# Kernel tuning notes

Measured on AMD Instinct MI355X. Metric: run time of the kernel, lower is better.

Reference implementation:

```python
import jax, jax.numpy as jnp
import numpy as np

NUM_NODES = 100000
NUM_EDGES = 600000
NUM_GRAPHS = 1000
EMB = 128


def setup_inputs() -> dict:
    key = jax.random.key(0)
    ks = jax.random.split(key, 12)
    x = jax.random.normal(ks[0], (NUM_NODES, 4), dtype=jnp.float32)
    edge_index = jax.random.randint(ks[1], (2, NUM_EDGES), 0, NUM_NODES, dtype=jnp.int32)
    x_scalar = jax.random.normal(ks[2], (NUM_GRAPHS, 4), dtype=jnp.float32)
    batch_index = jnp.sort(jax.random.randint(ks[3], (NUM_NODES,), 0, NUM_GRAPHS, dtype=jnp.int32))
    def glorot(k, shape):
        fan_in, fan_out = shape[0], shape[1]
        s = jnp.sqrt(2.0 / (fan_in + fan_out)).astype(jnp.float32)
        return jax.random.normal(k, shape, dtype=jnp.float32) * s
    return {
        "x": x,
        "edge_index": edge_index,
        "x_scalar": x_scalar,
        "batch_index": batch_index,
        "W0": glorot(ks[4], (4, EMB)), "b0": jnp.zeros((EMB,), jnp.float32),
        "W1": glorot(ks[5], (EMB, EMB)), "b1": jnp.zeros((EMB,), jnp.float32),
        "W2": glorot(ks[6], (EMB, EMB)), "b2": jnp.zeros((EMB,), jnp.float32),
        "W3": glorot(ks[7], (EMB, EMB)), "b3": jnp.zeros((EMB,), jnp.float32),
        "Wl1": glorot(ks[8], (EMB + 4, 64)), "bl1": jnp.zeros((64,), jnp.float32),
        "Wl2": glorot(ks[9], (64, 1)), "bl2": jnp.zeros((1,), jnp.float32),
    }


def _gcn_norm(edge_index, num_nodes):
    # PyG GCNConv default: add self-loops, symmetric normalization
    loop = jnp.arange(num_nodes, dtype=edge_index.dtype)
    src = jnp.concatenate([edge_index[0], loop])
    dst = jnp.concatenate([edge_index[1], loop])
    deg = jax.ops.segment_sum(jnp.ones_like(src, dtype=jnp.float32), dst,
                              num_segments=num_nodes)
    dinv = jnp.where(deg > 0, jax.lax.rsqrt(jnp.maximum(deg, 1e-12)), 0.0)
    norm = dinv[src] * dinv[dst]  # [E+N]
    return src, dst, norm


def _gcn_conv(h, src, dst, norm, W, b, num_nodes):
    h = h @ W                                   # [N, out]
    msg = h[src] * norm[:, None]                # gather + normalize
    out = jax.ops.segment_sum(msg, dst, num_segments=num_nodes)  # scatter-add
    return out + b


def reference(x, edge_index, x_scalar, batch_index,
              W0, b0, W1, b1, W2, b2, W3, b3, Wl1, bl1, Wl2, bl2):
    n = x.shape[0]
    src, dst, norm = _gcn_norm(edge_index, n)
    h = jax.nn.relu(_gcn_conv(x, src, dst, norm, W0, b0, n))
    h = jax.nn.relu(_gcn_conv(h, src, dst, norm, W1, b1, n))
    h = jax.nn.relu(_gcn_conv(h, src, dst, norm, W2, b2, n))
    h = jax.nn.relu(_gcn_conv(h, src, dst, norm, W3, b3, n))
    # global mean pool over batch_index
    sums = jax.ops.segment_sum(h, batch_index, num_segments=NUM_GRAPHS)
    cnts = jax.ops.segment_sum(jnp.ones((n,), jnp.float32), batch_index,
                               num_segments=NUM_GRAPHS)
    pooled = sums / jnp.maximum(cnts, 1.0)[:, None]          # [G, EMB]
    feat = jnp.concatenate([pooled, x_scalar], axis=1)       # [G, EMB+4]
    out = jax.nn.relu(feat @ Wl1 + bl1) @ Wl2 + bl2          # [G, 1]
    return out
```

## Files before the change

kernel.cpp:

```cpp
#include <hip/hip_runtime.h>

#define NN 100000
#define EE 600000
#define GG 1000
#define NB ((NN + 255) / 256)

typedef __bf16 bf16x8 __attribute__((ext_vector_type(8)));
typedef float f32x4 __attribute__((ext_vector_type(4)));
typedef unsigned int u32;

__device__ inline float2 bf2_to_f2(u32 u) {
  return make_float2(__uint_as_float(u << 16), __uint_as_float(u & 0xffff0000u));
}
__device__ inline u32 f2_to_bf2(float a, float b) {
  union { __bf16 h[2]; u32 u; } pk;
  pk.h[0] = (__bf16)a; pk.h[1] = (__bf16)b;
  return pk.u;
}


__global__ void k_init(int* cnt, int* fillc, int* gstart) {
  int i = blockIdx.x * 256 + threadIdx.x;
  if (i < NN) { cnt[i] = 0; fillc[i] = 0; }
  if (i <= GG) gstart[i] = NN;
}

__global__ void k_count(const int* __restrict__ dst, int* cnt) {
  int e = blockIdx.x * 256 + threadIdx.x;
  if (e < EE) atomicAdd(&cnt[dst[e]], 1);
}

__global__ void k_scan1(const int* __restrict__ cnt, float* __restrict__ dinv,
                        int* rowptr, int* bsum) {
  __shared__ int s[256];
  int tid = threadIdx.x;
  int i = blockIdx.x * 256 + tid;
  int v = (i < NN) ? ((cnt[i] + 7) & ~7) : 0;
  if (i < NN) dinv[i] = rsqrtf((float)(cnt[i] + 1));
  s[tid] = v;
  __syncthreads();
  for (int off = 1; off < 256; off <<= 1) {
    int t = (tid >= off) ? s[tid - off] : 0;
    __syncthreads();
    s[tid] += t;
    __syncthreads();
  }
  if (i <= NN) rowptr[i] = s[tid] - v;
  if (tid == 255) bsum[blockIdx.x] = s[255];
}

__global__ void k_scan2(int* bsum) {
  __shared__ int s[512];
  int tid = threadIdx.x;
  int v = (tid < NB) ? bsum[tid] : 0;
  s[tid] = v;
  __syncthreads();
  for (int off = 1; off < 512; off <<= 1) {
    int t = (tid >= off) ? s[tid - off] : 0;
    __syncthreads();
    s[tid] += t;
    __syncthreads();
  }
  if (tid < NB) bsum[tid] = s[tid] - v;
}

__global__ void k_scan3(int* rowptr, const int* __restrict__ bsum) {
  int i = blockIdx.x * 256 + threadIdx.x;
  if (i <= NN) rowptr[i] += bsum[blockIdx.x];
}

__global__ void k_fillpad(const int* __restrict__ src, const int* __restrict__ dst,
                          const int* __restrict__ rowptr, int* fillc,
                          const int* __restrict__ cnt,
                          const float* __restrict__ dinv,
                          int2* __restrict__ csr) {
  int gid = blockIdx.x * 256 + threadIdx.x;
  if (gid < EE) {
    int s = src[gid], d = dst[gid];
    int pos = rowptr[d] + atomicAdd(&fillc[d], 1);
    csr[pos] = make_int2(s, __float_as_int(dinv[s] * dinv[d]));
  }
  if (gid < NN) {
    int2 pad = make_int2(gid, 0);
    for (int pos = rowptr[gid] + cnt[gid]; pos < rowptr[gid + 1]; ++pos)
      csr[pos] = pad;
  }
}

__global__ void k_gbound(const int* __restrict__ batch, int* gstart) {
  int i = blockIdx.x * 256 + threadIdx.x;
  if (i >= NN) return;
  int b = batch[i];
  if (i == 0) {
    for (int g = 0; g <= b; ++g) gstart[g] = 0;
  } else {
    int prev = batch[i - 1];
    for (int g = prev + 1; g <= b; ++g) gstart[g] = i;
  }
}

__global__ void k_wprep(const float* __restrict__ W, __bf16* __restrict__ Wt) {
  int idx = blockIdx.x * 256 + threadIdx.x;
  int n = idx >> 7, k = idx & 127;
  Wt[(size_t)n * 128 + k] = (__bf16)W[(size_t)k * 128 + n];
}


__global__ void k_mm0(const float* __restrict__ x, const float* __restrict__ W0,
                      __bf16* __restrict__ hout) {
  int idx = blockIdx.x * 256 + threadIdx.x;
  if (idx >= NN * 128) return;
  int node = idx >> 7, j = idx & 127;
  const float* xr = x + node * 4;
  float s = xr[0] * W0[j];
  s = fmaf(xr[1], W0[128 + j], s);
  s = fmaf(xr[2], W0[256 + j], s);
  s = fmaf(xr[3], W0[384 + j], s);
  hout[idx] = (__bf16)s;
}

#define LDSPAD 136
__global__ __launch_bounds__(256) void k_mfma(const __bf16* __restrict__ hin,
                                              const __bf16* __restrict__ Wt,
                                              __bf16* __restrict__ hout) {
  __shared__ __bf16 As[128 * LDSPAD];
  int tid = threadIdx.x;
  int row0 = blockIdx.x * 128;
  int lane = tid & 63, w = tid >> 6;
  int ln = lane & 15, quad = lane >> 4;

  bf16x8 bfrag[8][4];
  #pragma unroll
  for (int nt = 0; nt < 8; ++nt)
    #pragma unroll
    for (int kc = 0; kc < 4; ++kc)
      bfrag[nt][kc] = *(const bf16x8*)(Wt + (size_t)(nt * 16 + ln) * 128 + kc * 32 + quad * 8);

  #pragma unroll
  for (int i = 0; i < 8; ++i) {
    int eb = (i * 256 + tid) * 8;
    int r = eb >> 7, c = eb & 127;
    int gr = row0 + r;
    uint4 v = make_uint4(0, 0, 0, 0);
    if (gr < NN) v = *(const uint4*)(hin + (size_t)gr * 128 + c);
    *(uint4*)&As[r * LDSPAD + c] = v;
  }
  __syncthreads();

  f32x4 acc[2][8];
  #pragma unroll
  for (int rt = 0; rt < 2; ++rt)
    #pragma unroll
    for (int nt = 0; nt < 8; ++nt) acc[rt][nt] = (f32x4){0.f, 0.f, 0.f, 0.f};

  #pragma unroll
  for (int kc = 0; kc < 4; ++kc) {
    bf16x8 a0 = *(const bf16x8*)&As[(w * 32 + ln) * LDSPAD + kc * 32 + quad * 8];
    bf16x8 a1 = *(const bf16x8*)&As[(w * 32 + 16 + ln) * LDSPAD + kc * 32 + quad * 8];
    #pragma unroll
    for (int nt = 0; nt < 8; ++nt) {
      acc[0][nt] = __builtin_amdgcn_mfma_f32_16x16x32_bf16(a0, bfrag[nt][kc], acc[0][nt], 0, 0, 0);
      acc[1][nt] = __builtin_amdgcn_mfma_f32_16x16x32_bf16(a1, bfrag[nt][kc], acc[1][nt], 0, 0, 0);
    }
  }

  #pragma unroll
  for (int rt = 0; rt < 2; ++rt)
    #pragma unroll
    for (int nt = 0; nt < 8; ++nt)
      #pragma unroll
      for (int reg = 0; reg < 4; ++reg) {
        int gr = row0 + w * 32 + rt * 16 + quad * 4 + reg;
        if (gr < NN)
          hout[(size_t)gr * 128 + nt * 16 + ln] = (__bf16)acc[rt][nt][reg];
      }
}

__global__ __launch_bounds__(256) void k_aggregate(const __bf16* __restrict__ hlin,
                                                   const int* __restrict__ rowptr,
                                                   const int2* __restrict__ csr,
                                                   const float* __restrict__ dinv,
                                                   const float* __restrict__ bias,
                                                   u32* __restrict__ hout2) {
  int node = blockIdx.x * 4 + (threadIdx.x >> 6);
  int lane = threadIdx.x & 63;
  int ln = lane & 15, quad = lane >> 4;
  if (node >= NN) return;
  float di = dinv[node];
  float sw = di * di;

  uint4 su = *(const uint4*)(hlin + ((size_t)node << 7) + ln * 8);
  float4 ba = *(const float4*)(bias + ln * 8);
  float4 bb = *(const float4*)(bias + ln * 8 + 4);
  float2 s0 = bf2_to_f2(su.x), s1 = bf2_to_f2(su.y);
  float2 s2 = bf2_to_f2(su.z), s3 = bf2_to_f2(su.w);
  float q0 = (quad == 0) ? 1.f : 0.f;
  float acc[8];
  acc[0] = q0 * fmaf(sw, s0.x, ba.x); acc[1] = q0 * fmaf(sw, s0.y, ba.y);
  acc[2] = q0 * fmaf(sw, s1.x, ba.z); acc[3] = q0 * fmaf(sw, s1.y, ba.w);
  acc[4] = q0 * fmaf(sw, s2.x, bb.x); acc[5] = q0 * fmaf(sw, s2.y, bb.y);
  acc[6] = q0 * fmaf(sw, s3.x, bb.z); acc[7] = q0 * fmaf(sw, s3.y, bb.w);

  int beg = rowptr[node], end = rowptr[node + 1];
  for (int base = beg; base < end; base += 64) {
    int m = end - base; if (m > 64) m = 64;
    int li = base + (lane < m ? lane : m - 1);
    int2 md = csr[li];
    int idxv = md.x, wbits = md.y;
    for (int j = 0; j < m; j += 8) {
      int sl0 = (j + quad) * 4, sl1 = (j + 4 + quad) * 4;
      int r0 = __builtin_amdgcn_ds_bpermute(sl0, idxv);
      int r1 = __builtin_amdgcn_ds_bpermute(sl1, idxv);
      float w0 = __int_as_float(__builtin_amdgcn_ds_bpermute(sl0, wbits));
      float w1 = __int_as_float(__builtin_amdgcn_ds_bpermute(sl1, wbits));
      uint4 u0 = *(const uint4*)(hlin + ((size_t)r0 << 7) + ln * 8);
      uint4 u1 = *(const uint4*)(hlin + ((size_t)r1 << 7) + ln * 8);
      float2 f;
      f = bf2_to_f2(u0.x); acc[0] = fmaf(w0, f.x, acc[0]); acc[1] = fmaf(w0, f.y, acc[1]);
      f = bf2_to_f2(u0.y); acc[2] = fmaf(w0, f.x, acc[2]); acc[3] = fmaf(w0, f.y, acc[3]);
      f = bf2_to_f2(u0.z); acc[4] = fmaf(w0, f.x, acc[4]); acc[5] = fmaf(w0, f.y, acc[5]);
      f = bf2_to_f2(u0.w); acc[6] = fmaf(w0, f.x, acc[6]); acc[7] = fmaf(w0, f.y, acc[7]);
      f = bf2_to_f2(u1.x); acc[0] = fmaf(w1, f.x, acc[0]); acc[1] = fmaf(w1, f.y, acc[1]);
      f = bf2_to_f2(u1.y); acc[2] = fmaf(w1, f.x, acc[2]); acc[3] = fmaf(w1, f.y, acc[3]);
      f = bf2_to_f2(u1.z); acc[4] = fmaf(w1, f.x, acc[4]); acc[5] = fmaf(w1, f.y, acc[5]);
      f = bf2_to_f2(u1.w); acc[6] = fmaf(w1, f.x, acc[6]); acc[7] = fmaf(w1, f.y, acc[7]);
    }
  }

  #pragma unroll
  for (int k = 0; k < 8; ++k) {
    acc[k] += __shfl_xor(acc[k], 16);
    acc[k] += __shfl_xor(acc[k], 32);
  }
  if (quad == 0) {
    uint4 o;
    o.x = f2_to_bf2(fmaxf(acc[0], 0.f), fmaxf(acc[1], 0.f));
    o.y = f2_to_bf2(fmaxf(acc[2], 0.f), fmaxf(acc[3], 0.f));
    o.z = f2_to_bf2(fmaxf(acc[4], 0.f), fmaxf(acc[5], 0.f));
    o.w = f2_to_bf2(fmaxf(acc[6], 0.f), fmaxf(acc[7], 0.f));
    *(uint4*)(hout2 + (size_t)node * 64 + ln * 4) = o;
  }
}

__global__ __launch_bounds__(256) void k_poolmlp(const uint2* __restrict__ h4u,
                                                 const int* __restrict__ gstart,
                                                 const float* __restrict__ xs,
                                                 const float* __restrict__ Wl1,
                                                 const float* __restrict__ bl1,
                                                 const float* __restrict__ Wl2,
                                                 const float* __restrict__ bl2,
                                                 float* __restrict__ out) {
  __shared__ float4 part[8][32];
  __shared__ float pooled[128];
  int g = blockIdx.x;
  int beg = gstart[g], end = gstart[g + 1];
  int tid = threadIdx.x;
  int cg = tid & 31;
  int rg = tid >> 5;
  float4 acc = make_float4(0.f, 0.f, 0.f, 0.f);
  for (int i = beg + rg; i < end; i += 8) {
    uint2 u = h4u[(size_t)i * 32 + cg];
    acc.x += __uint_as_float(u.x << 16);
    acc.y += __uint_as_float(u.x & 0xffff0000u);
    acc.z += __uint_as_float(u.y << 16);
    acc.w += __uint_as_float(u.y & 0xffff0000u);
  }
  part[rg][cg] = acc;
  __syncthreads();
  if (tid < 32) {
    float4 s = part[0][tid];
    #pragma unroll
    for (int r = 1; r < 8; ++r) {
      float4 v = part[r][tid];
      s.x += v.x; s.y += v.y; s.z += v.z; s.w += v.w;
    }
    float sc = 1.f / fmaxf((float)(end - beg), 1.f);
    pooled[tid * 4 + 0] = s.x * sc;
    pooled[tid * 4 + 1] = s.y * sc;
    pooled[tid * 4 + 2] = s.z * sc;
    pooled[tid * 4 + 3] = s.w * sc;
  }
  __syncthreads();
  if (tid < 64) {
    float hj = bl1[tid];
    #pragma unroll 4
    for (int k = 0; k < 128; ++k) hj = fmaf(pooled[k], Wl1[k * 64 + tid], hj);
    const float* xr = xs + g * 4;
    #pragma unroll
    for (int k = 0; k < 4; ++k) hj = fmaf(xr[k], Wl1[(128 + k) * 64 + tid], hj);
    hj = fmaxf(hj, 0.f);
    float val = hj * Wl2[tid];
    #pragma unroll
    for (int off = 32; off > 0; off >>= 1) val += __shfl_down(val, off);
    if (tid == 0) out[g] = val + bl2[0];
  }
}


extern "C" void kernel_launch(void* const* d_in, const int* in_sizes, int n_in,
                              void* d_out, int out_size, void* d_ws, size_t ws_size,
                              hipStream_t stream) {
  const float* x    = (const float*)d_in[0];
  const int*   ei   = (const int*)d_in[1];
  const float* xs   = (const float*)d_in[2];
  const int*   batch= (const int*)d_in[3];
  const float* W0   = (const float*)d_in[4];
  const float* b0   = (const float*)d_in[5];
  const float* W1   = (const float*)d_in[6];
  const float* b1   = (const float*)d_in[7];
  const float* W2   = (const float*)d_in[8];
  const float* b2   = (const float*)d_in[9];
  const float* W3   = (const float*)d_in[10];
  const float* b3   = (const float*)d_in[11];
  const float* Wl1  = (const float*)d_in[12];
  const float* bl1  = (const float*)d_in[13];
  const float* Wl2  = (const float*)d_in[14];
  const float* bl2  = (const float*)d_in[15];
  const int* srcA = ei;
  const int* dstA = ei + EE;
  float* out = (float*)d_out;

  char* p = (char*)d_ws;
  auto take = [&](size_t bytes) { char* q = p; p += (bytes + 255) & ~(size_t)255; return q; };
  __bf16* hA   = (__bf16*)take((size_t)NN * 128 * 2);
  __bf16* hB   = (__bf16*)take((size_t)NN * 128 * 2);
  int*   cnt   = (int*)take((size_t)NN * 4);
  float* dinv  = (float*)take((size_t)NN * 4);
  int*   rowptr= (int*)take((size_t)(NN + 1) * 4);
  int*   fillc = (int*)take((size_t)NN * 4);
  int2*  csr   = (int2*)take((size_t)(EE + 7 * NN + 64) * 8);
  int*   bsum  = (int*)take(512 * 4);
  int*   gstart= (int*)take((size_t)(GG + 1) * 4);
  __bf16* Wt1  = (__bf16*)take(16384 * 2);
  __bf16* Wt2  = (__bf16*)take(16384 * 2);
  __bf16* Wt3  = (__bf16*)take(16384 * 2);

  k_init<<<NB, 256, 0, stream>>>(cnt, fillc, gstart);
  k_count<<<(EE + 255) / 256, 256, 0, stream>>>(dstA, cnt);
  k_scan1<<<NB, 256, 0, stream>>>(cnt, dinv, rowptr, bsum);
  k_scan2<<<1, 512, 0, stream>>>(bsum);
  k_scan3<<<NB, 256, 0, stream>>>(rowptr, bsum);
  k_fillpad<<<(EE + 255) / 256, 256, 0, stream>>>(srcA, dstA, rowptr, fillc, cnt, dinv, csr);
  k_gbound<<<NB, 256, 0, stream>>>(batch, gstart);
  k_wprep<<<64, 256, 0, stream>>>(W1, Wt1);
  k_wprep<<<64, 256, 0, stream>>>(W2, Wt2);
  k_wprep<<<64, 256, 0, stream>>>(W3, Wt3);

  k_mm0<<<(NN * 128 + 255) / 256, 256, 0, stream>>>(x, W0, hA);
  k_aggregate<<<(NN + 3) / 4, 256, 0, stream>>>(hA, rowptr, csr, dinv, b0, (u32*)hB);
  k_mfma<<<(NN + 127) / 128, 256, 0, stream>>>(hB, Wt1, hA);
  k_aggregate<<<(NN + 3) / 4, 256, 0, stream>>>(hA, rowptr, csr, dinv, b1, (u32*)hB);
  k_mfma<<<(NN + 127) / 128, 256, 0, stream>>>(hB, Wt2, hA);
  k_aggregate<<<(NN + 3) / 4, 256, 0, stream>>>(hA, rowptr, csr, dinv, b2, (u32*)hB);
  k_mfma<<<(NN + 127) / 128, 256, 0, stream>>>(hB, Wt3, hA);
  k_aggregate<<<(NN + 3) / 4, 256, 0, stream>>>(hA, rowptr, csr, dinv, b3, (u32*)hB);

  k_poolmlp<<<GG, 256, 0, stream>>>((const uint2*)hB, gstart, xs, Wl1, bl1, Wl2, bl2, out);
}
```

Baseline: 414.2 us.

## Aggregate before linear transform so first layer gathers 4-wide input

Reorders each GCN layer to aggregate neighbours first and then apply the weight matrix, moving bias and ReLU into the MFMA epilogue. The first layer now gathers the 4-feature input instead of 128-wide transformed features, removing one full 128-wide sparse aggregation pass. Setup kernels for CSR fill, graph bounds and weight transposes are merged into one launch. Rounding points for bf16 intermediates change slightly.

```diff
diff --git a/kernel.cpp b/kernel.cpp
--- a/kernel.cpp
+++ b/kernel.cpp
@@ -69,11 +69,16 @@
   if (i <= NN) rowptr[i] += bsum[blockIdx.x];
 }
 
-__global__ void k_fillpad(const int* __restrict__ src, const int* __restrict__ dst,
-                          const int* __restrict__ rowptr, int* fillc,
-                          const int* __restrict__ cnt,
-                          const float* __restrict__ dinv,
-                          int2* __restrict__ csr) {
+__global__ void k_setup2(const int* __restrict__ src, const int* __restrict__ dst,
+                         const int* __restrict__ rowptr, int* fillc,
+                         const int* __restrict__ cnt,
+                         const float* __restrict__ dinv,
+                         int2* __restrict__ csr,
+                         const int* __restrict__ batch, int* gstart,
+                         const float* __restrict__ W1, const float* __restrict__ W2,
+                         const float* __restrict__ W3,
+                         __bf16* __restrict__ Wt1, __bf16* __restrict__ Wt2,
+                         __bf16* __restrict__ Wt3) {
   int gid = blockIdx.x * 256 + threadIdx.x;
   if (gid < EE) {
     int s = src[gid], d = dst[gid];
@@ -84,44 +89,64 @@
     int2 pad = make_int2(gid, 0);
     for (int pos = rowptr[gid] + cnt[gid]; pos < rowptr[gid + 1]; ++pos)
       csr[pos] = pad;
-  }
-}
-
-__global__ void k_gbound(const int* __restrict__ batch, int* gstart) {
+    int b = batch[gid];
+    if (gid == 0) {
+      for (int g = 0; g <= b; ++g) gstart[g] = 0;
+    } else {
+      int prev = batch[gid - 1];
+      for (int g = prev + 1; g <= b; ++g) gstart[g] = gid;
+    }
+  }
+  if (gid < 3 * 16384) {
+    int which = gid >> 14, idx = gid & 16383;
+    int n = idx >> 7, k = idx & 127;
+    const float* W = (which == 0) ? W1 : (which == 1) ? W2 : W3;
+    __bf16* Wt = (which == 0) ? Wt1 : (which == 1) ? Wt2 : Wt3;
+    Wt[(size_t)n * 128 + k] = (__bf16)W[(size_t)k * 128 + n];
+  }
+}
+
+
+__global__ void k_aggx(const float4* __restrict__ x, const int* __restrict__ rowptr,
+                       const int* __restrict__ cnt, const int2* __restrict__ csr,
+                       const float* __restrict__ dinv, float4* __restrict__ y) {
   int i = blockIdx.x * 256 + threadIdx.x;
   if (i >= NN) return;
-  int b = batch[i];
-  if (i == 0) {
-    for (int g = 0; g <= b; ++g) gstart[g] = 0;
-  } else {
-    int prev = batch[i - 1];
-    for (int g = prev + 1; g <= b; ++g) gstart[g] = i;
-  }
-}
-
-__global__ void k_wprep(const float* __restrict__ W, __bf16* __restrict__ Wt) {
-  int idx = blockIdx.x * 256 + threadIdx.x;
-  int n = idx >> 7, k = idx & 127;
-  Wt[(size_t)n * 128 + k] = (__bf16)W[(size_t)k * 128 + n];
-}
-
-
-__global__ void k_mm0(const float* __restrict__ x, const float* __restrict__ W0,
-                      __bf16* __restrict__ hout) {
+  float di = dinv[i];
+  float sw = di * di;
+  float4 xi = x[i];
+  float4 acc = make_float4(sw * xi.x, sw * xi.y, sw * xi.z, sw * xi.w);
+  int beg = rowptr[i], end = beg + cnt[i];
+  for (int e = beg; e < end; ++e) {
+    int2 md = csr[e];
+    float w = __int_as_float(md.y);
+    float4 v = x[md.x];
+    acc.x = fmaf(w, v.x, acc.x);
+    acc.y = fmaf(w, v.y, acc.y);
+    acc.z = fmaf(w, v.z, acc.z);
+    acc.w = fmaf(w, v.w, acc.w);
+  }
+  y[i] = acc;
+}
+
+__global__ void k_lin0(const float4* __restrict__ y, const float* __restrict__ W0,
+                       const float* __restrict__ b0, __bf16* __restrict__ hout) {
   int idx = blockIdx.x * 256 + threadIdx.x;
   if (idx >= NN * 128) return;
   int node = idx >> 7, j = idx & 127;
-  const float* xr = x + node * 4;
-  float s = xr[0] * W0[j];
-  s = fmaf(xr[1], W0[128 + j], s);
-  s = fmaf(xr[2], W0[256 + j], s);
-  s = fmaf(xr[3], W0[384 + j], s);
-  hout[idx] = (__bf16)s;
+  float4 yv = y[node];
+  float s = b0[j];
+  s = fmaf(yv.x, W0[j], s);
+  s = fmaf(yv.y, W0[128 + j], s);
+  s = fmaf(yv.z, W0[256 + j], s);
+  s = fmaf(yv.w, W0[384 + j], s);
+  hout[idx] = (__bf16)fmaxf(s, 0.f);
 }
 
 #define LDSPAD 136
 __global__ __launch_bounds__(256) void k_mfma(const __bf16* __restrict__ hin,
                                               const __bf16* __restrict__ Wt,
+                                              const float* __restrict__ bias,
                                               __bf16* __restrict__ hout) {
   __shared__ __bf16 As[128 * LDSPAD];
   int tid = threadIdx.x;
@@ -130,11 +155,14 @@
   int ln = lane & 15, quad = lane >> 4;
 
   bf16x8 bfrag[8][4];
-  #pragma unroll
-  for (int nt = 0; nt < 8; ++nt)
+  float bcol[8];
+  #pragma unroll
+  for (int nt = 0; nt < 8; ++nt) {
+    bcol[nt] = bias[nt * 16 + ln];
     #pragma unroll
     for (int kc = 0; kc < 4; ++kc)
       bfrag[nt][kc] = *(const bf16x8*)(Wt + (size_t)(nt * 16 + ln) * 128 + kc * 32 + quad * 8);
+  }
 
   #pragma unroll
   for (int i = 0; i < 8; ++i) {
@@ -172,7 +200,8 @@
       for (int reg = 0; reg < 4; ++reg) {
         int gr = row0 + w * 32 + rt * 16 + quad * 4 + reg;
         if (gr < NN)
-          hout[(size_t)gr * 128 + nt * 16 + ln] = (__bf16)acc[rt][nt][reg];
+          hout[(size_t)gr * 128 + nt * 16 + ln] =
+              (__bf16)fmaxf(acc[rt][nt][reg] + bcol[nt], 0.f);
       }
 }
 
@@ -180,7 +209,6 @@
                                                    const int* __restrict__ rowptr,
                                                    const int2* __restrict__ csr,
                                                    const float* __restrict__ dinv,
-                                                   const float* __restrict__ bias,
                                                    u32* __restrict__ hout2) {
   int node = blockIdx.x * 4 + (threadIdx.x >> 6);
   int lane = threadIdx.x & 63;
@@ -190,16 +218,14 @@
   float sw = di * di;
 
   uint4 su = *(const uint4*)(hlin + ((size_t)node << 7) + ln * 8);
-  float4 ba = *(const float4*)(bias + ln * 8);
-  float4 bb = *(const float4*)(bias + ln * 8 + 4);
   float2 s0 = bf2_to_f2(su.x), s1 = bf2_to_f2(su.y);
   float2 s2 = bf2_to_f2(su.z), s3 = bf2_to_f2(su.w);
-  float q0 = (quad == 0) ? 1.f : 0.f;
+  float q0 = (quad == 0) ? sw : 0.f;
   float acc[8];
-  acc[0] = q0 * fmaf(sw, s0.x, ba.x); acc[1] = q0 * fmaf(sw, s0.y, ba.y);
-  acc[2] = q0 * fmaf(sw, s1.x, ba.z); acc[3] = q0 * fmaf(sw, s1.y, ba.w);
-  acc[4] = q0 * fmaf(sw, s2.x, bb.x); acc[5] = q0 * fmaf(sw, s2.y, bb.y);
-  acc[6] = q0 * fmaf(sw, s3.x, bb.z); acc[7] = q0 * fmaf(sw, s3.y, bb.w);
+  acc[0] = q0 * s0.x; acc[1] = q0 * s0.y;
+  acc[2] = q0 * s1.x; acc[3] = q0 * s1.y;
+  acc[4] = q0 * s2.x; acc[5] = q0 * s2.y;
+  acc[6] = q0 * s3.x; acc[7] = q0 * s3.y;
 
   int beg = rowptr[node], end = rowptr[node + 1];
   for (int base = beg; base < end; base += 64) {
@@ -234,10 +260,10 @@
   }
   if (quad == 0) {
     uint4 o;
-    o.x = f2_to_bf2(fmaxf(acc[0], 0.f), fmaxf(acc[1], 0.f));
-    o.y = f2_to_bf2(fmaxf(acc[2], 0.f), fmaxf(acc[3], 0.f));
-    o.z = f2_to_bf2(fmaxf(acc[4], 0.f), fmaxf(acc[5], 0.f));
-    o.w = f2_to_bf2(fmaxf(acc[6], 0.f), fmaxf(acc[7], 0.f));
+    o.x = f2_to_bf2(acc[0], acc[1]);
+    o.y = f2_to_bf2(acc[2], acc[3]);
+    o.z = f2_to_bf2(acc[4], acc[5]);
+    o.w = f2_to_bf2(acc[6], acc[7]);
     *(uint4*)(hout2 + (size_t)node * 64 + ln * 4) = o;
   }
 }
@@ -324,6 +350,7 @@
   auto take = [&](size_t bytes) { char* q = p; p += (bytes + 255) & ~(size_t)255; return q; };
   __bf16* hA   = (__bf16*)take((size_t)NN * 128 * 2);
   __bf16* hB   = (__bf16*)take((size_t)NN * 128 * 2);
+  float*  y    = (float*)take((size_t)NN * 4 * 4);
   int*   cnt   = (int*)take((size_t)NN * 4);
   float* dinv  = (float*)take((size_t)NN * 4);
   int*   rowptr= (int*)take((size_t)(NN + 1) * 4);
@@ -340,20 +367,18 @@
   k_scan1<<<NB, 256, 0, stream>>>(cnt, dinv, rowptr, bsum);
   k_scan2<<<1, 512, 0, stream>>>(bsum);
   k_scan3<<<NB, 256, 0, stream>>>(rowptr, bsum);
-  k_fillpad<<<(EE + 255) / 256, 256, 0, stream>>>(srcA, dstA, rowptr, fillc, cnt, dinv, csr);
-  k_gbound<<<NB, 256, 0, stream>>>(batch, gstart);
-  k_wprep<<<64, 256, 0, stream>>>(W1, Wt1);
-  k_wprep<<<64, 256, 0, stream>>>(W2, Wt2);
-  k_wprep<<<64, 256, 0, stream>>>(W3, Wt3);
-
-  k_mm0<<<(NN * 128 + 255) / 256, 256, 0, stream>>>(x, W0, hA);
-  k_aggregate<<<(NN + 3) / 4, 256, 0, stream>>>(hA, rowptr, csr, dinv, b0, (u32*)hB);
-  k_mfma<<<(NN + 127) / 128, 256, 0, stream>>>(hB, Wt1, hA);
-  k_aggregate<<<(NN + 3) / 4, 256, 0, stream>>>(hA, rowptr, csr, dinv, b1, (u32*)hB);
-  k_mfma<<<(NN + 127) / 128, 256, 0, stream>>>(hB, Wt2, hA);
-  k_aggregate<<<(NN + 3) / 4, 256, 0, stream>>>(hA, rowptr, csr, dinv, b2, (u32*)hB);
-  k_mfma<<<(NN + 127) / 128, 256, 0, stream>>>(hB, Wt3, hA);
-  k_aggregate<<<(NN + 3) / 4, 256, 0, stream>>>(hA, rowptr, csr, dinv, b3, (u32*)hB);
-
-  k_poolmlp<<<GG, 256, 0, stream>>>((const uint2*)hB, gstart, xs, Wl1, bl1, Wl2, bl2, out);
-}
+  k_setup2<<<(EE + 255) / 256, 256, 0, stream>>>(srcA, dstA, rowptr, fillc, cnt, dinv,
+                                                 csr, batch, gstart, W1, W2, W3,
+                                                 Wt1, Wt2, Wt3);
+
+  k_aggx<<<NB, 256, 0, stream>>>((const float4*)x, rowptr, cnt, csr, dinv, (float4*)y);
+  k_lin0<<<(NN * 128 + 255) / 256, 256, 0, stream>>>((const float4*)y, W0, b0, hA);
+  k_aggregate<<<(NN + 3) / 4, 256, 0, stream>>>(hA, rowptr, csr, dinv, (u32*)hB);
+  k_mfma<<<(NN + 127) / 128, 256, 0, stream>>>(hB, Wt1, b1, hA);
+  k_aggregate<<<(NN + 3) / 4, 256, 0, stream>>>(hA, rowptr, csr, dinv, (u32*)hB);
+  k_mfma<<<(NN + 127) / 128, 256, 0, stream>>>(hB, Wt2, b2, hA);
+  k_aggregate<<<(NN + 3) / 4, 256, 0, stream>>>(hA, rowptr, csr, dinv, (u32*)hB);
+  k_mfma<<<(NN + 127) / 128, 256, 0, stream>>>(hB, Wt3, b3, hA);
+
+  k_poolmlp<<<GG, 256, 0, stream>>>((const uint2*)hA, gstart, xs, Wl1, bl1, Wl2, bl2, out);
+}
```

Result: faster. 381.0 us (-8.0%).
